# Performance work log

Hardware: AMD Instinct MI355X
Metric: run time of the kernel (lower is better)

## Reference

```python
import jax, jax.numpy as jnp
import numpy as np

N_EMBD = 2048
N_HEAD = 16
HEAD_DIM = N_EMBD // N_HEAD
B, T = 8, 1024
EPS = 1e-5


def setup_inputs() -> dict:
    key = jax.random.key(0)
    ks = jax.random.split(key, 8)
    s = 0.02
    return {
        "x": jax.random.normal(ks[0], (B, T, N_EMBD), dtype=jnp.float32),
        "ln1_w": jnp.ones((N_EMBD,), jnp.float32),
        "ln1_b": jnp.zeros((N_EMBD,), jnp.float32),
        "qkv_w": jax.random.normal(ks[1], (3 * N_EMBD, N_EMBD), jnp.float32) * s,
        "qkv_b": jnp.zeros((3 * N_EMBD,), jnp.float32),
        "out_w": jax.random.normal(ks[2], (N_EMBD, N_EMBD), jnp.float32) * s,
        "out_b": jnp.zeros((N_EMBD,), jnp.float32),
        "ln2_w": jnp.ones((N_EMBD,), jnp.float32),
        "ln2_b": jnp.zeros((N_EMBD,), jnp.float32),
        "fc1_w": jax.random.normal(ks[3], (4 * N_EMBD, N_EMBD), jnp.float32) * s,
        "fc1_b": jnp.zeros((4 * N_EMBD,), jnp.float32),
        "fc2_w": jax.random.normal(ks[4], (N_EMBD, 4 * N_EMBD), jnp.float32) * s,
        "fc2_b": jnp.zeros((N_EMBD,), jnp.float32),
    }


def _layernorm(x, w, b):
    mu = jnp.mean(x, axis=-1, keepdims=True)
    var = jnp.var(x, axis=-1, keepdims=True)
    return (x - mu) * jax.lax.rsqrt(var + EPS) * w + b


def _attention(x, qkv_w, qkv_b, out_w, out_b):
    Bb, Tt, C = x.shape
    qkv = x @ qkv_w.T + qkv_b                      # [B,T,3C]
    q, k, v = jnp.split(qkv, 3, axis=-1)
    def heads(t):  # [B,T,C] -> [B,H,T,D]
        return t.reshape(Bb, Tt, N_HEAD, HEAD_DIM).transpose(0, 2, 1, 3)
    q, k, v = heads(q), heads(k), heads(v)
    scale = 1.0 / np.sqrt(HEAD_DIM).astype(np.float32)
    scores = jnp.einsum('bhqd,bhkd->bhqk', q, k) * scale
    causal = jnp.tril(jnp.ones((Tt, Tt), dtype=bool))
    scores = jnp.where(causal, scores, -jnp.inf)
    attn = jax.nn.softmax(scores, axis=-1)         # dropout p=0 -> identity
    out = jnp.einsum('bhqk,bhkd->bhqd', attn, v)
    out = out.transpose(0, 2, 1, 3).reshape(Bb, Tt, C)
    return out @ out_w.T + out_b


def _mlp(x, fc1_w, fc1_b, fc2_w, fc2_b):
    h = jax.nn.gelu(x @ fc1_w.T + fc1_b, approximate=False)  # torch GELU is exact erf
    return h @ fc2_w.T + fc2_b


def reference(x, ln1_w, ln1_b, qkv_w, qkv_b, out_w, out_b,
              ln2_w, ln2_b, fc1_w, fc1_b, fc2_w, fc2_b):
    x = x + _attention(_layernorm(x, ln1_w, ln1_b), qkv_w, qkv_b, out_w, out_b)
    x = x + _mlp(_layernorm(x, ln2_w, ln2_b), fc1_w, fc1_b, fc2_w, fc2_b)
    return x
```

## Files before the change

kernel.cpp:

```cpp
#include <hip/hip_runtime.h>
#include <hip/hip_bf16.h>

typedef __attribute__((ext_vector_type(8))) short short8;
typedef __attribute__((ext_vector_type(4))) short short4v;
typedef __attribute__((ext_vector_type(4))) float f32x4;
typedef __attribute__((address_space(3))) char lds_char;

static __device__ __forceinline__ ushort f2bf(float f) {
  union { __hip_bfloat16 h; ushort u; } cv;
  cv.h = __float2bfloat16(f);
  return cv.u;
}

#define GLOAD_LDS16(gp, lp)                                            \
  __builtin_amdgcn_global_load_lds(                                    \
      (const __attribute__((address_space(1))) void*)(gp),             \
      (__attribute__((address_space(3))) void*)(lp), 16, 0, 0)

#define BAR   asm volatile("s_barrier" ::: "memory")
#define VM0   asm volatile("s_waitcnt vmcnt(0)" ::: "memory")
#define VM6   asm volatile("s_waitcnt vmcnt(6)" ::: "memory")
#define LGKM0_SB do { asm volatile("s_waitcnt lgkmcnt(0)" ::: "memory");  \
                      __builtin_amdgcn_sched_barrier(0); } while (0)

__global__ __launch_bounds__(256) void cvt_all_k(const float* __restrict__ w0, ushort* __restrict__ o0, int n0,
                                                 const float* __restrict__ w1, ushort* __restrict__ o1, int n1,
                                                 const float* __restrict__ w2, ushort* __restrict__ o2, int n2,
                                                 const float* __restrict__ w3, ushort* __restrict__ o3, int n3) {
  int i = blockIdx.x * 256 + threadIdx.x;
  const float* in; ushort* out;
  if (i < n0)           { in = w0; out = o0; }
  else if (i < n0 + n1) { i -= n0; in = w1; out = o1; }
  else if (i < n0 + n1 + n2) { i -= n0 + n1; in = w2; out = o2; }
  else                  { i -= n0 + n1 + n2; if (i >= n3) return; in = w3; out = o3; }
  const float4* p = (const float4*)in + (size_t)i * 2;
  float4 a = p[0], b = p[1];
  short8 o;
  o[0] = f2bf(a.x); o[1] = f2bf(a.y); o[2] = f2bf(a.z); o[3] = f2bf(a.w);
  o[4] = f2bf(b.x); o[5] = f2bf(b.y); o[6] = f2bf(b.z); o[7] = f2bf(b.w);
  ((short8*)out)[i] = o;
}

__global__ __launch_bounds__(256) void ln_k(const float* __restrict__ x, const float* __restrict__ w,
                                            const float* __restrict__ b, ushort* __restrict__ o) {
  const int row = blockIdx.x, t = threadIdx.x;
  const float* xr = x + (size_t)row * 2048;
  float4 v0 = *(const float4*)(xr + t * 4);
  float4 v1 = *(const float4*)(xr + t * 4 + 1024);
  float s  = v0.x + v0.y + v0.z + v0.w + v1.x + v1.y + v1.z + v1.w;
  float s2 = v0.x*v0.x + v0.y*v0.y + v0.z*v0.z + v0.w*v0.w
           + v1.x*v1.x + v1.y*v1.y + v1.z*v1.z + v1.w*v1.w;
  #pragma unroll
  for (int m = 32; m; m >>= 1) { s += __shfl_xor(s, m); s2 += __shfl_xor(s2, m); }
  __shared__ float red[8];
  const int lane = t & 63, wv = t >> 6;
  if (lane == 0) { red[wv * 2] = s; red[wv * 2 + 1] = s2; }
  __syncthreads();
  s  = red[0] + red[2] + red[4] + red[6];
  s2 = red[1] + red[3] + red[5] + red[7];
  const float mu = s * (1.f / 2048.f);
  const float rstd = rsqrtf(s2 * (1.f / 2048.f) - mu * mu + 1e-5f);
  float4 w0 = *(const float4*)(w + t * 4), w1 = *(const float4*)(w + t * 4 + 1024);
  float4 b0 = *(const float4*)(b + t * 4), b1 = *(const float4*)(b + t * 4 + 1024);
  short4v o0, o1;
  o0[0] = f2bf((v0.x - mu) * rstd * w0.x + b0.x);
  o0[1] = f2bf((v0.y - mu) * rstd * w0.y + b0.y);
  o0[2] = f2bf((v0.z - mu) * rstd * w0.z + b0.z);
  o0[3] = f2bf((v0.w - mu) * rstd * w0.w + b0.w);
  o1[0] = f2bf((v1.x - mu) * rstd * w1.x + b1.x);
  o1[1] = f2bf((v1.y - mu) * rstd * w1.y + b1.y);
  o1[2] = f2bf((v1.z - mu) * rstd * w1.z + b1.z);
  o1[3] = f2bf((v1.w - mu) * rstd * w1.w + b1.w);
  *(short4v*)(o + (size_t)row * 2048 + t * 4) = o0;
  *(short4v*)(o + (size_t)row * 2048 + t * 4 + 1024) = o1;
}

template <int EPI>
__global__ __launch_bounds__(512) void gemm256_k(const ushort* __restrict__ A, const ushort* __restrict__ B,
                                                 const float* __restrict__ bias, const float* __restrict__ res,
                                                 void* __restrict__ outp, int M, int N, int K) {
  __shared__ __align__(16) char lds[2][65536];
  const int nbn = N >> 8;
  const int nwg = gridDim.x;
  const int cpx = nwg >> 3;
  const int bid = (blockIdx.x & 7) * cpx + (blockIdx.x >> 3);
  const int gsz = nbn << 2;
  const int g = bid / gsz, rr = bid % gsz;
  const int bm = (g << 2) + (rr & 3), bn = rr >> 2;
  const int m0 = bm << 8, n0 = bn << 8;
  const int t = threadIdx.x, lane = t & 63, wid = t >> 6;
  const int wr = wid >> 2, wcn = wid & 3;
  const int hi = lane >> 4, lo = lane & 15;
  const int srow = lane >> 3, sc8 = lane & 7;
  const int gcs = (sc8 ^ srow) * 8;
  const ushort* Abase = A + (size_t)m0 * K;
  const ushort* Bbase = B + (size_t)n0 * K;
  f32x4 acc[8][4] = {};
  short8 a[4][2], b0[2][2], b1[2][2];

  auto stage = [&](int buf, int mat, int h, int tt) {
    const ushort* G = mat ? Bbase : Abase;
    char* L = (char*)lds[buf] + mat * 32768;
    const size_t kof = (size_t)tt * 64 + gcs;
    #pragma unroll
    for (int j = 0; j < 2; j++) {
      const int rb = h * 128 + wid * 16 + j * 8;
      GLOAD_LDS16(G + (size_t)(rb + srow) * K + kof, (ushort*)(L + rb * 128));
    }
  };
  auto rdA = [&](const char* LA, int MP, short8 af[4][2]) {
    #pragma unroll
    for (int m = 0; m < 4; m++) {
      const int row = MP * 128 + wr * 64 + m * 16 + lo;
      const int sz = (row & 7) << 4;
      #pragma unroll
      for (int kk = 0; kk < 2; kk++)
        af[m][kk] = *(const short8*)(LA + row * 128 + ((kk * 64 + hi * 16) ^ sz));
    }
  };
  auto rdB = [&](const char* LB, int NP, short8 bq[2][2]) {
    #pragma unroll
    for (int n = 0; n < 2; n++) {
      const int row = NP * 128 + wcn * 32 + n * 16 + lo;
      const int sz = (row & 7) << 4;
      #pragma unroll
      for (int kk = 0; kk < 2; kk++)
        bq[n][kk] = *(const short8*)(LB + row * 128 + ((kk * 64 + hi * 16) ^ sz));
    }
  };
  auto mfma16 = [&](int MP, int NP, short8 af[4][2], short8 bq[2][2]) {
    __builtin_amdgcn_s_setprio(1);
    #pragma unroll
    for (int m = 0; m < 4; m++)
      #pragma unroll
      for (int n = 0; n < 2; n++) {
        acc[MP*4+m][NP*2+n] = __builtin_amdgcn_mfma_f32_16x16x32_bf16(af[m][0], bq[n][0], acc[MP*4+m][NP*2+n], 0, 0, 0);
        acc[MP*4+m][NP*2+n] = __builtin_amdgcn_mfma_f32_16x16x32_bf16(af[m][1], bq[n][1], acc[MP*4+m][NP*2+n], 0, 0, 0);
      }
    __builtin_amdgcn_s_setprio(0);
  };

  const int NT = K >> 6, NI = NT >> 1;
  stage(0, 0, 0, 0); stage(0, 1, 0, 0); stage(0, 1, 1, 0); stage(0, 0, 1, 0);
  stage(1, 0, 0, 1); stage(1, 1, 0, 1); stage(1, 1, 1, 1);
  VM6; BAR;

  const char* LA0 = (const char*)lds[0]; const char* LB0 = (const char*)lds[0] + 32768;
  const char* LA1 = (const char*)lds[1]; const char* LB1 = (const char*)lds[1] + 32768;

  for (int i = 0; i < NI; ++i) {
    const int u = 2 * i;
    const bool lastI = (i == NI - 1);
    rdA(LA0, 0, a); rdB(LB0, 0, b0);
    stage(1, 0, 1, u + 1);
    BAR; mfma16(0, 0, a, b0);
    rdB(LB0, 1, b1);
    BAR; mfma16(0, 1, a, b1);
    rdA(LA0, 1, a);
    if (!lastI) { stage(0, 0, 0, u + 2); stage(0, 1, 0, u + 2); }
    BAR; mfma16(1, 1, a, b1);
    if (!lastI) stage(0, 1, 1, u + 2);
    if (lastI) { VM0; } else { VM6; }
    BAR; mfma16(1, 0, a, b0);
    rdA(LA1, 0, a); rdB(LB1, 0, b0);
    if (!lastI) stage(0, 0, 1, u + 2);
    BAR; mfma16(0, 0, a, b0);
    rdB(LB1, 1, b1);
    BAR; mfma16(0, 1, a, b1);
    rdA(LA1, 1, a);
    if (!lastI) { stage(1, 0, 0, u + 3); stage(1, 1, 0, u + 3); }
    BAR; mfma16(1, 1, a, b1);
    if (!lastI) { stage(1, 1, 1, u + 3); VM6; }
    BAR; mfma16(1, 0, a, b0);
  }

  #pragma unroll
  for (int mi = 0; mi < 8; mi++) {
    const int grow = m0 + (mi >> 2) * 128 + wr * 64 + (mi & 3) * 16 + hi * 4;
    #pragma unroll
    for (int ni = 0; ni < 4; ni++) {
      const int gcol = n0 + (ni >> 1) * 128 + wcn * 32 + (ni & 1) * 16 + lo;
      const float bv = bias[gcol];
      #pragma unroll
      for (int r = 0; r < 4; r++) {
        const size_t idx = (size_t)(grow + r) * N + gcol;
        float v = acc[mi][ni][r] + bv;
        if constexpr (EPI == 0) ((ushort*)outp)[idx] = f2bf(v);
        else if constexpr (EPI == 1) ((float*)outp)[idx] = res[idx] + v;
        else if constexpr (EPI == 2) ((ushort*)outp)[idx] = f2bf(0.5f * v * (1.f + erff(v * 0.70710678118f)));
        else ((float*)outp)[idx] += v;
      }
    }
  }
}

__global__ __launch_bounds__(256) void attn_k(const ushort* __restrict__ qkv, ushort* __restrict__ o) {
  const int qb = 15 - blockIdx.y;
  const int bh = blockIdx.x;
  const int bb = bh >> 4, h = bh & 15;
  const int t = threadIdx.x, lane = t & 63, w = t >> 6;
  const int hi = lane >> 4, lo = lane & 15;
  __shared__ __align__(16) char ldsK[64 * 256];
  __shared__ __align__(16) char ldsV[64 * 256];
  __shared__ __align__(16) char ldsP[4][16 * 128];
  const size_t base = (size_t)bb * 1024 * 6144;
  const int qrow_a = qb * 64 + w * 16 + lo;
  short8 qf[4];
  #pragma unroll
  for (int kk = 0; kk < 4; kk++)
    qf[kk] = *(const short8*)(qkv + base + (size_t)qrow_a * 6144 + h * 128 + kk * 32 + hi * 8);
  float ms[4], ls[4];
  f32x4 oacc[8] = {};
  #pragma unroll
  for (int r = 0; r < 4; r++) { ms[r] = -1e30f; ls[r] = 0.f; }
  const int wave_qmax = qb * 64 + w * 16 + 15;
  const uint vbase = (uint)(size_t)(lds_char*)ldsV + hi * 2048 + lo * 8;
  const int k_r4  = lane >> 4;
  const int v_kv4 = (lane >> 1) & 3;
  const int v_d0  = (lane >> 3) * 16 + (lane & 1) * 8;

  for (int kv0 = 0; kv0 <= qb * 64; kv0 += 64) {
    __syncthreads();
    #pragma unroll
    for (int j = 0; j < 4; j++) {
      const int rb = w * 16 + j * 4;
      const int r  = rb + k_r4;
      const int c16 = (lane & 15) ^ (r & 7);
      GLOAD_LDS16(qkv + base + (size_t)(kv0 + r) * 6144 + 2048 + h * 128 + c16 * 8,
                  ldsK + rb * 256);
    }
    #pragma unroll
    for (int j = 0; j < 4; j++) {
      const int g = w * 4 + j;
      GLOAD_LDS16(qkv + base + (size_t)(kv0 + g * 4 + v_kv4) * 6144 + 4096 + h * 128 + v_d0,
                  ldsV + g * 1024);
    }
    __syncthreads();
    if (kv0 > wave_qmax) continue;
    f32x4 s[4];
    #pragma unroll
    for (int nb = 0; nb < 4; nb++) {
      f32x4 z = {};
      const int krow = nb * 16 + lo;
      #pragma unroll
      for (int kk = 0; kk < 4; kk++) {
        const int cb = kk * 64 + hi * 16;
        short8 kf = *(const short8*)(ldsK + krow * 256 + (cb ^ ((krow & 7) << 4)));
        z = __builtin_amdgcn_mfma_f32_16x16x32_bf16(qf[kk], kf, z, 0, 0, 0);
      }
      s[nb] = z;
    }
    float corr[4];
    #pragma unroll
    for (int r = 0; r < 4; r++) {
      const int qrow = qb * 64 + w * 16 + hi * 4 + r;
      float mx = -1e30f;
      #pragma unroll
      for (int nb = 0; nb < 4; nb++) {
        const int kcol = kv0 + nb * 16 + lo;
        float sv = s[nb][r] * 0.08838834764831845f;
        sv = (kcol <= qrow) ? sv : -1e30f;
        s[nb][r] = sv;
        mx = fmaxf(mx, sv);
      }
      #pragma unroll
      for (int msk = 1; msk < 16; msk <<= 1) mx = fmaxf(mx, __shfl_xor(mx, msk));
      const float mnew = fmaxf(ms[r], mx);
      corr[r] = __expf(ms[r] - mnew);
      ms[r] = mnew;
      float rs = 0.f;
      #pragma unroll
      for (int nb = 0; nb < 4; nb++) {
        const float p = __expf(s[nb][r] - mnew);
        s[nb][r] = p; rs += p;
      }
      #pragma unroll
      for (int msk = 1; msk < 16; msk <<= 1) rs += __shfl_xor(rs, msk);
      ls[r] = ls[r] * corr[r] + rs;
    }
    #pragma unroll
    for (int nf = 0; nf < 8; nf++)
      #pragma unroll
      for (int r = 0; r < 4; r++) oacc[nf][r] *= corr[r];
    #pragma unroll
    for (int r = 0; r < 4; r++) {
      const int prow = hi * 4 + r;
      #pragma unroll
      for (int nb = 0; nb < 4; nb++) {
        const int pcol = nb * 16 + lo;
        *(short*)(ldsP[w] + prow * 128 + ((pcol * 2) ^ ((prow & 7) << 4))) = (short)f2bf(s[nb][r]);
      }
    }
    #pragma unroll
    for (int ks = 0; ks < 2; ks++) {
      short8 pf = *(const short8*)(ldsP[w] + lo * 128 + ((ks * 64 + hi * 16) ^ ((lo & 7) << 4)));
      short4v v0[8], v1[8];
      #pragma unroll
      for (int nf = 0; nf < 8; nf++) {
        const uint a0 = vbase + ks * 8192 + nf * 128;
        asm volatile("ds_read_b64_tr_b16 %0, %1" : "=v"(v0[nf]) : "v"(a0));
        asm volatile("ds_read_b64_tr_b16 %0, %1" : "=v"(v1[nf]) : "v"(a0 + 1024));
      }
      LGKM0_SB;
      #pragma unroll
      for (int nf = 0; nf < 8; nf++) {
        short8 vf = __builtin_shufflevector(v0[nf], v1[nf], 0, 1, 2, 3, 4, 5, 6, 7);
        oacc[nf] = __builtin_amdgcn_mfma_f32_16x16x32_bf16(pf, vf, oacc[nf], 0, 0, 0);
      }
    }
  }
  #pragma unroll
  for (int r = 0; r < 4; r++) {
    const float inv = 1.f / ls[r];
    const int qrow = qb * 64 + w * 16 + hi * 4 + r;
    ushort* orow = o + ((size_t)(bb * 1024 + qrow)) * 2048 + h * 128;
    #pragma unroll
    for (int nf = 0; nf < 8; nf++)
      orow[nf * 16 + lo] = f2bf(oacc[nf][r] * inv);
  }
}

extern "C" void kernel_launch(void* const* d_in, const int* in_sizes, int n_in,
                              void* d_out, int out_size, void* d_ws, size_t ws_size,
                              hipStream_t stream) {
  const float* x     = (const float*)d_in[0];
  const float* ln1w  = (const float*)d_in[1];
  const float* ln1b  = (const float*)d_in[2];
  const float* qkvw  = (const float*)d_in[3];
  const float* qkvb  = (const float*)d_in[4];
  const float* outw  = (const float*)d_in[5];
  const float* outb  = (const float*)d_in[6];
  const float* ln2w  = (const float*)d_in[7];
  const float* ln2b  = (const float*)d_in[8];
  const float* fc1w  = (const float*)d_in[9];
  const float* fc1b  = (const float*)d_in[10];
  const float* fc2w  = (const float*)d_in[11];
  const float* fc2b  = (const float*)d_in[12];
  float* out = (float*)d_out;

  char* ws = (char*)d_ws;
  ushort* qkvw_bf = (ushort*)(ws);
  ushort* outw_bf = (ushort*)(ws + 25165824);
  ushort* fc1w_bf = (ushort*)(ws + 33554432);
  ushort* fc2w_bf = (ushort*)(ws + 67108864);
  ushort* bufA    = (ushort*)(ws + 100663296);
  ushort* bufR    = (ushort*)(ws + 134217728);

  cvt_all_k<<<24576, 256, 0, stream>>>(qkvw, qkvw_bf, 1572864,
                                       outw, outw_bf, 524288,
                                       fc1w, fc1w_bf, 2097152,
                                       fc2w, fc2w_bf, 2097152);

  ln_k<<<8192, 256, 0, stream>>>(x, ln1w, ln1b, bufA);
  gemm256_k<0><<<32 * 24, 512, 0, stream>>>(bufA, qkvw_bf, qkvb, nullptr, bufR, 8192, 6144, 2048);
  attn_k<<<dim3(128, 16), 256, 0, stream>>>(bufR, bufA);
  gemm256_k<1><<<32 * 8, 512, 0, stream>>>(bufA, outw_bf, outb, x, out, 8192, 2048, 2048);
  ln_k<<<8192, 256, 0, stream>>>(out, ln2w, ln2b, bufA);
  gemm256_k<2><<<32 * 32, 512, 0, stream>>>(bufA, fc1w_bf, fc1b, nullptr, bufR, 8192, 8192, 2048);
  gemm256_k<3><<<32 * 8, 512, 0, stream>>>(bufR, fc2w_bf, fc2b, nullptr, out, 8192, 2048, 8192);
}
```

Measured before the change: 962.3 us.

## Shrink GEMM tile to 256x128 with single-buffered LDS for occupancy

The GEMM kernel moves from a 256x256 tile with a double-buffered, interleaved 8-phase pipeline to a 256x128 tile with a single 48KB LDS buffer and a simple load-wait-compute loop. Launch bounds now request more resident workgroups, and the grids double. The intent is higher occupancy and more workgroups so that latency is hidden by other waves rather than by explicit software pipelining. In exchange, each tile reuses less data (more global and LDS traffic per FLOP), and every K step fully exposes its load latency within the workgroup.

After: 1.010 ms. 1.05x slower.

```diff
diff --git a/kernel.cpp b/kernel.cpp
--- a/kernel.cpp
+++ b/kernel.cpp
@@ -19,7 +19,6 @@
 
 #define BAR   asm volatile("s_barrier" ::: "memory")
 #define VM0   asm volatile("s_waitcnt vmcnt(0)" ::: "memory")
-#define VM6   asm volatile("s_waitcnt vmcnt(6)" ::: "memory")
 #define LGKM0_SB do { asm volatile("s_waitcnt lgkmcnt(0)" ::: "memory");  \
                       __builtin_amdgcn_sched_barrier(0); } while (0)
 
@@ -76,18 +75,18 @@
 }
 
 template <int EPI>
-__global__ __launch_bounds__(512) void gemm256_k(const ushort* __restrict__ A, const ushort* __restrict__ B,
-                                                 const float* __restrict__ bias, const float* __restrict__ res,
-                                                 void* __restrict__ outp, int M, int N, int K) {
-  __shared__ __align__(16) char lds[2][65536];
-  const int nbn = N >> 8;
+__global__ __launch_bounds__(512, 4) void gemm256_k(const ushort* __restrict__ A, const ushort* __restrict__ B,
+                                                    const float* __restrict__ bias, const float* __restrict__ res,
+                                                    void* __restrict__ outp, int M, int N, int K) {
+  __shared__ __align__(16) char lds[49152];
+  const int nbn = N >> 7;
   const int nwg = gridDim.x;
   const int cpx = nwg >> 3;
   const int bid = (blockIdx.x & 7) * cpx + (blockIdx.x >> 3);
   const int gsz = nbn << 2;
   const int g = bid / gsz, rr = bid % gsz;
   const int bm = (g << 2) + (rr & 3), bn = rr >> 2;
-  const int m0 = bm << 8, n0 = bn << 8;
+  const int m0 = bm << 8, n0 = bn << 7;
   const int t = threadIdx.x, lane = t & 63, wid = t >> 6;
   const int wr = wid >> 2, wcn = wid & 3;
   const int hi = lane >> 4, lo = lane & 15;
@@ -95,96 +94,65 @@
   const int gcs = (sc8 ^ srow) * 8;
   const ushort* Abase = A + (size_t)m0 * K;
   const ushort* Bbase = B + (size_t)n0 * K;
-  f32x4 acc[8][4] = {};
-  short8 a[4][2], b0[2][2], b1[2][2];
-
-  auto stage = [&](int buf, int mat, int h, int tt) {
-    const ushort* G = mat ? Bbase : Abase;
-    char* L = (char*)lds[buf] + mat * 32768;
+  f32x4 acc[8][2] = {};
+
+  auto stageA = [&](int h, int tt) {
     const size_t kof = (size_t)tt * 64 + gcs;
     #pragma unroll
     for (int j = 0; j < 2; j++) {
       const int rb = h * 128 + wid * 16 + j * 8;
-      GLOAD_LDS16(G + (size_t)(rb + srow) * K + kof, (ushort*)(L + rb * 128));
+      GLOAD_LDS16(Abase + (size_t)(rb + srow) * K + kof, (ushort*)(lds + rb * 128));
     }
   };
-  auto rdA = [&](const char* LA, int MP, short8 af[4][2]) {
-    #pragma unroll
-    for (int m = 0; m < 4; m++) {
-      const int row = MP * 128 + wr * 64 + m * 16 + lo;
-      const int sz = (row & 7) << 4;
-      #pragma unroll
-      for (int kk = 0; kk < 2; kk++)
-        af[m][kk] = *(const short8*)(LA + row * 128 + ((kk * 64 + hi * 16) ^ sz));
+  auto stageB = [&](int tt) {
+    const size_t kof = (size_t)tt * 64 + gcs;
+    #pragma unroll
+    for (int j = 0; j < 2; j++) {
+      const int rb = wid * 16 + j * 8;
+      GLOAD_LDS16(Bbase + (size_t)(rb + srow) * K + kof, (ushort*)(lds + 32768 + rb * 128));
     }
   };
-  auto rdB = [&](const char* LB, int NP, short8 bq[2][2]) {
-    #pragma unroll
-    for (int n = 0; n < 2; n++) {
-      const int row = NP * 128 + wcn * 32 + n * 16 + lo;
-      const int sz = (row & 7) << 4;
-      #pragma unroll
-      for (int kk = 0; kk < 2; kk++)
-        bq[n][kk] = *(const short8*)(LB + row * 128 + ((kk * 64 + hi * 16) ^ sz));
-    }
-  };
-  auto mfma16 = [&](int MP, int NP, short8 af[4][2], short8 bq[2][2]) {
+
+  const int swz = (lo & 7) << 4;
+  const char* LA = lds;
+  const char* LB = lds + 32768;
+  const int arow0 = wr * 128 + lo;
+  const int brow0 = wcn * 32 + lo;
+
+  const int NT = K >> 6;
+  stageA(0, 0); stageA(1, 0); stageB(0);
+
+  for (int tt = 0; tt < NT; ++tt) {
+    VM0; BAR;
     __builtin_amdgcn_s_setprio(1);
     #pragma unroll
-    for (int m = 0; m < 4; m++)
-      #pragma unroll
-      for (int n = 0; n < 2; n++) {
-        acc[MP*4+m][NP*2+n] = __builtin_amdgcn_mfma_f32_16x16x32_bf16(af[m][0], bq[n][0], acc[MP*4+m][NP*2+n], 0, 0, 0);
-        acc[MP*4+m][NP*2+n] = __builtin_amdgcn_mfma_f32_16x16x32_bf16(af[m][1], bq[n][1], acc[MP*4+m][NP*2+n], 0, 0, 0);
-      }
+    for (int kk = 0; kk < 2; kk++) {
+      const int cb = kk * 64 + hi * 16;
+      short8 bb0 = *(const short8*)(LB + (brow0 + 0)  * 128 + (cb ^ swz));
+      short8 bb1 = *(const short8*)(LB + (brow0 + 16) * 128 + (cb ^ swz));
+      #pragma unroll
+      for (int m = 0; m < 8; m++) {
+        short8 af = *(const short8*)(LA + (arow0 + m * 16) * 128 + (cb ^ swz));
+        acc[m][0] = __builtin_amdgcn_mfma_f32_16x16x32_bf16(af, bb0, acc[m][0], 0, 0, 0);
+        acc[m][1] = __builtin_amdgcn_mfma_f32_16x16x32_bf16(af, bb1, acc[m][1], 0, 0, 0);
+      }
+    }
     __builtin_amdgcn_s_setprio(0);
-  };
-
-  const int NT = K >> 6, NI = NT >> 1;
-  stage(0, 0, 0, 0); stage(0, 1, 0, 0); stage(0, 1, 1, 0); stage(0, 0, 1, 0);
-  stage(1, 0, 0, 1); stage(1, 1, 0, 1); stage(1, 1, 1, 1);
-  VM6; BAR;
-
-  const char* LA0 = (const char*)lds[0]; const char* LB0 = (const char*)lds[0] + 32768;
-  const char* LA1 = (const char*)lds[1]; const char* LB1 = (const char*)lds[1] + 32768;
-
-  for (int i = 0; i < NI; ++i) {
-    const int u = 2 * i;
-    const bool lastI = (i == NI - 1);
-    rdA(LA0, 0, a); rdB(LB0, 0, b0);
-    stage(1, 0, 1, u + 1);
-    BAR; mfma16(0, 0, a, b0);
-    rdB(LB0, 1, b1);
-    BAR; mfma16(0, 1, a, b1);
-    rdA(LA0, 1, a);
-    if (!lastI) { stage(0, 0, 0, u + 2); stage(0, 1, 0, u + 2); }
-    BAR; mfma16(1, 1, a, b1);
-    if (!lastI) stage(0, 1, 1, u + 2);
-    if (lastI) { VM0; } else { VM6; }
-    BAR; mfma16(1, 0, a, b0);
-    rdA(LA1, 0, a); rdB(LB1, 0, b0);
-    if (!lastI) stage(0, 0, 1, u + 2);
-    BAR; mfma16(0, 0, a, b0);
-    rdB(LB1, 1, b1);
-    BAR; mfma16(0, 1, a, b1);
-    rdA(LA1, 1, a);
-    if (!lastI) { stage(1, 0, 0, u + 3); stage(1, 1, 0, u + 3); }
-    BAR; mfma16(1, 1, a, b1);
-    if (!lastI) { stage(1, 1, 1, u + 3); VM6; }
-    BAR; mfma16(1, 0, a, b0);
+    BAR;
+    if (tt + 1 < NT) { stageA(0, tt + 1); stageA(1, tt + 1); stageB(tt + 1); }
   }
 
   #pragma unroll
-  for (int mi = 0; mi < 8; mi++) {
-    const int grow = m0 + (mi >> 2) * 128 + wr * 64 + (mi & 3) * 16 + hi * 4;
-    #pragma unroll
-    for (int ni = 0; ni < 4; ni++) {
-      const int gcol = n0 + (ni >> 1) * 128 + wcn * 32 + (ni & 1) * 16 + lo;
+  for (int m = 0; m < 8; m++) {
+    const int grow = m0 + wr * 128 + m * 16 + hi * 4;
+    #pragma unroll
+    for (int ni = 0; ni < 2; ni++) {
+      const int gcol = n0 + wcn * 32 + ni * 16 + lo;
       const float bv = bias[gcol];
       #pragma unroll
       for (int r = 0; r < 4; r++) {
         const size_t idx = (size_t)(grow + r) * N + gcol;
-        float v = acc[mi][ni][r] + bv;
+        float v = acc[m][ni][r] + bv;
         if constexpr (EPI == 0) ((ushort*)outp)[idx] = f2bf(v);
         else if constexpr (EPI == 1) ((float*)outp)[idx] = res[idx] + v;
         else if constexpr (EPI == 2) ((ushort*)outp)[idx] = f2bf(0.5f * v * (1.f + erff(v * 0.70710678118f)));
@@ -352,10 +320,10 @@
                                        fc2w, fc2w_bf, 2097152);
 
   ln_k<<<8192, 256, 0, stream>>>(x, ln1w, ln1b, bufA);
-  gemm256_k<0><<<32 * 24, 512, 0, stream>>>(bufA, qkvw_bf, qkvb, nullptr, bufR, 8192, 6144, 2048);
+  gemm256_k<0><<<1536, 512, 0, stream>>>(bufA, qkvw_bf, qkvb, nullptr, bufR, 8192, 6144, 2048);
   attn_k<<<dim3(128, 16), 256, 0, stream>>>(bufR, bufA);
-  gemm256_k<1><<<32 * 8, 512, 0, stream>>>(bufA, outw_bf, outb, x, out, 8192, 2048, 2048);
+  gemm256_k<1><<<512, 512, 0, stream>>>(bufA, outw_bf, outb, x, out, 8192, 2048, 2048);
   ln_k<<<8192, 256, 0, stream>>>(out, ln2w, ln2b, bufA);
-  gemm256_k<2><<<32 * 32, 512, 0, stream>>>(bufA, fc1w_bf, fc1b, nullptr, bufR, 8192, 8192, 2048);
-  gemm256_k<3><<<32 * 8, 512, 0, stream>>>(bufR, fc2w_bf, fc2b, nullptr, out, 8192, 2048, 8192);
-}
+  gemm256_k<2><<<2048, 512, 0, stream>>>(bufA, fc1w_bf, fc1b, nullptr, bufR, 8192, 8192, 2048);
+  gemm256_k<3><<<512, 512, 0, stream>>>(bufR, fc2w_bf, fc2b, nullptr, out, 8192, 2048, 8192);
+}
```
